# Kernel tuning notes

Measured on AMD Instinct MI355X. Metric: run time of the kernel, lower is better.

The kernel has to match this reference:

```python
import jax, jax.numpy as jnp
import numpy as np

NTOKEN, NINP, NHID = 50257, 256, 256
B, T = 64, 2048
RES, FC1 = 10, NHID // 3
EPS = 1e-5

def lrelu(x, p=0.01):
    return jnp.maximum(x, x * p)

def setup_inputs() -> dict:
    key = jax.random.key(0)
    ks = jax.random.split(key, 12)
    s = 0.05
    inp = {
        "input": jax.random.randint(ks[0], (B, T), 0, NTOKEN),
        "hx": jnp.zeros((B, NHID), jnp.float32),
        "cx": jnp.zeros((B, NHID), jnp.float32),
        "seq_len": jax.random.randint(ks[1], (B,), 1, T + 1),  # lengths in [1, T]
        "emb_w": jax.random.uniform(ks[2], (NTOKEN, NINP), jnp.float32, -0.1, 0.1),
        "W_ih": jax.random.normal(ks[3], (4 * NHID, NINP), jnp.float32) * s,
        "W_hh": jax.random.normal(ks[4], (4 * NHID, NHID), jnp.float32) * s,
        "b_ih": jnp.zeros((4 * NHID,), jnp.float32),
        "b_hh": jnp.zeros((4 * NHID,), jnp.float32),
        "rfc1_w": jax.random.normal(ks[5], (RES, NHID), jnp.float32) * s,
        "rfc1_b": jnp.zeros((RES,), jnp.float32),
        "rbn_g": jnp.ones((RES,), jnp.float32),
        "rbn_b": jnp.zeros((RES,), jnp.float32),
        "rbn_rm": jnp.zeros((RES,), jnp.float32),
        "rbn_rv": jnp.ones((RES,), jnp.float32),
        "rfc2_w": jax.random.normal(ks[6], (NHID, RES), jnp.float32) * s,
        "rfc2_b": jnp.zeros((NHID,), jnp.float32),
        "fc1_w": jax.random.normal(ks[7], (FC1, NHID), jnp.float32) * s,
        "fc1_b": jnp.zeros((FC1,), jnp.float32),
        "bn1_g": jnp.ones((FC1,), jnp.float32),
        "bn1_b": jnp.zeros((FC1,), jnp.float32),
        "bn1_rm": jnp.zeros((FC1,), jnp.float32),
        "bn1_rv": jnp.ones((FC1,), jnp.float32),
        "fc2_w": jax.random.normal(ks[8], (2, FC1), jnp.float32) * s,
        "fc2_b": jnp.zeros((2,), jnp.float32),
    }
    return inp

def reference(input, hx, cx, seq_len, emb_w, W_ih, W_hh, b_ih, b_hh,
              rfc1_w, rfc1_b, rbn_g, rbn_b, rbn_rm, rbn_rv, rfc2_w, rfc2_b,
              fc1_w, fc1_b, bn1_g, bn1_b, bn1_rm, bn1_rv, fc2_w, fc2_b):
    # eval mode: dropout = identity, noise = 0, BatchNorm uses running stats
    emb = emb_w[input.T]  # [T, B, ninp]
    # precompute input-side gates once (batched matmul) -> [T, B, 4*nhid]
    x_gates = jnp.einsum('tbi,gi->tbg', emb, W_ih) + b_ih + b_hh

    def step(carry, xg):
        h, c = carry
        gates = xg + h @ W_hh.T
        i, f, g, o = jnp.split(gates, 4, axis=-1)
        c = jax.nn.sigmoid(f) * c + jax.nn.sigmoid(i) * jnp.tanh(g)
        h = jax.nn.sigmoid(o) * jnp.tanh(c)
        return (h, c), h

    (hx_f, cx_f), outs = jax.lax.scan(step, (hx, cx), x_gates)  # outs: [T, B, nhid]

    # ragged mean pooling over first seq_len[b] steps
    mask = (jnp.arange(T)[:, None] < seq_len[None, :]).astype(outs.dtype)  # [T, B]
    feature = jnp.einsum('tbh,tb->bh', outs, mask) / seq_len[:, None].astype(outs.dtype)

    # ResNet block (eval)
    res = jax.nn.relu(feature) @ rfc1_w.T + rfc1_b
    res = jax.nn.relu(res)
    res = (res - rbn_rm) * jax.lax.rsqrt(rbn_rv + EPS) * rbn_g + rbn_b
    feature = feature + res @ rfc2_w.T + rfc2_b

    # classifier head
    fc = feature @ fc1_w.T + fc1_b
    fc = (fc - bn1_rm) * jax.lax.rsqrt(bn1_rv + EPS) * bn1_g + bn1_b
    fc = lrelu(fc)
    logits = fc @ fc2_w.T + fc2_b
    logp = jax.nn.log_softmax(logits, axis=-1)
    return (logp, hx_f, cx_f)
```

## Files before the change

kernel.cpp:

```cpp
#include <hip/hip_runtime.h>
#include <cstdint>


#define NTOKEN 50257
#define NINP 256
#define NHID 256
#define BB 64
#define TT 2048
#define NRES 10
#define NFC1 85
#define EPSV 1e-5f

typedef _Float16 f16;
typedef _Float16 f16x2 __attribute__((ext_vector_type(2)));
typedef _Float16 f16x8 __attribute__((ext_vector_type(8)));
typedef float f32x4 __attribute__((ext_vector_type(4)));

static __device__ __forceinline__ float sigm(float x) { return 1.0f / (1.0f + __expf(-x)); }
static __device__ __forceinline__ float tanh_(float x) {
  float ax = fabsf(x);
  float e = __expf(-2.0f * ax);
  float t = (1.0f - e) / (1.0f + e);
  return x < 0.0f ? -t : t;
}

static __device__ __forceinline__ float fdot2(f16x2 a, f16x2 b, float c) {
#if __has_builtin(__builtin_amdgcn_fdot2)
  return __builtin_amdgcn_fdot2(a, b, c, false);
#else
  return c + (float)a[0] * (float)b[0] + (float)a[1] * (float)b[1];
#endif
}

__global__ void k0_convert(const float* __restrict__ emb_w, const float* __restrict__ W_ih,
                           const float* __restrict__ b_ih, const float* __restrict__ b_hh,
                           f16* __restrict__ emb16, f16* __restrict__ wih16,
                           float* __restrict__ bias) {
  int64_t i = (int64_t)blockIdx.x * blockDim.x + threadIdx.x;
  if (i < (int64_t)NTOKEN * NINP) emb16[i] = (f16)emb_w[i];
  if (i < 4 * NHID * NINP) wih16[i] = (f16)W_ih[i];
  if (i < 4 * NHID) bias[i] = b_ih[i] + b_hh[i];
}

__global__ __launch_bounds__(256) void k1_gemm(const f16* __restrict__ emb16,
                                               const f16* __restrict__ wih16,
                                               const float* __restrict__ bias,
                                               f16* __restrict__ xgtab) {
  __shared__ __align__(16) f16 a_lds[64][40];
  __shared__ __align__(16) f16 b_lds[256][40];
  const int mt = blockIdx.x;
  const int nt0 = blockIdx.y * 256;
  const int tid = threadIdx.x;
  const int lane = tid & 63;
  const int w = tid >> 6;
  const int quad = lane >> 4;
  const int l16 = lane & 15;

  f32x4 acc[16];
#pragma unroll
  for (int i = 0; i < 16; i++) acc[i] = (f32x4){0.f, 0.f, 0.f, 0.f};

  const int ar = tid >> 2;
  int av = mt * 64 + ar;
  if (av > NTOKEN - 1) av = NTOKEN - 1;
  const int ac = (tid & 3) * 8;

  for (int kb = 0; kb < 256; kb += 32) {
    *(uint4*)&a_lds[ar][ac] = *(const uint4*)&emb16[av * 256 + kb + ac];
    {
      const uint4* bs = (const uint4*)&wih16[(nt0 + tid) * 256 + kb];
      uint4* bd = (uint4*)&b_lds[tid][0];
      bd[0] = bs[0]; bd[1] = bs[1]; bd[2] = bs[2]; bd[3] = bs[3];
    }
    __syncthreads();
    f16x8 af = *(const f16x8*)&a_lds[w * 16 + l16][quad * 8];
#pragma unroll
    for (int nt = 0; nt < 16; nt++) {
      f16x8 bf = *(const f16x8*)&b_lds[nt * 16 + l16][quad * 8];
      acc[nt] = __builtin_amdgcn_mfma_f32_16x16x32_f16(af, bf, acc[nt], 0, 0, 0);
    }
    __syncthreads();
  }
#pragma unroll
  for (int nt = 0; nt < 16; nt++) {
#pragma unroll
    for (int rg = 0; rg < 4; rg++) {
      int v = mt * 64 + w * 16 + quad * 4 + rg;
      if (v < NTOKEN) {
        int n = nt0 + nt * 16 + l16;
        xgtab[v * 1024 + n] = (f16)(acc[nt][rg] + bias[n]);
      }
    }
  }
}

#define RK 92
#define LK 36
__global__ __launch_bounds__(512, 2) void k2_rnn(
    const int* __restrict__ input, const float* __restrict__ hx0,
    const float* __restrict__ cx0, const int* __restrict__ seq_len,
    const float* __restrict__ Whh, const f16* __restrict__ xgtab,
    float* __restrict__ feat, float* __restrict__ out_hx, float* __restrict__ out_cx) {
  __shared__ uint2 lw2[LK * 512];
  __shared__ __align__(16) f16 hpak[NHID];
  __shared__ float fo_f[NHID];
  __shared__ float fo_o[NHID];

  const int b = blockIdx.x;
  const int tid = threadIdx.x;
  const int r0 = tid, r1 = tid + 512;

  unsigned int w0[RK], w1[RK];
#pragma unroll
  for (int m = 0; m < 128; m++) {
    float2 a = *(const float2*)&Whh[r0 * 256 + 2 * m];
    float2 d = *(const float2*)&Whh[r1 * 256 + 2 * m];
    f16x2 pa; pa[0] = (f16)a.x; pa[1] = (f16)a.y;
    f16x2 pd; pd[0] = (f16)d.x; pd[1] = (f16)d.y;
    unsigned int ua = __builtin_bit_cast(unsigned int, pa);
    unsigned int ud = __builtin_bit_cast(unsigned int, pd);
    if (m < RK) { w0[m] = ua; w1[m] = ud; }
    else { lw2[(m - RK) * 512 + tid] = make_uint2(ua, ud); }
  }

  float c = 0.0f, pool = 0.0f, hnew = 0.0f;
  if (tid < NHID) {
    hpak[tid] = (f16)hx0[b * NHID + tid];
    c = cx0[b * NHID + tid];
  }
  const int L = seq_len[b];
  __syncthreads();

  const int* tokp = input + b * TT;
  int tok_next = tokp[1];
  f16 xga, xgb;
  {
    int tok0 = tokp[0];
    xga = xgtab[tok0 * 1024 + r0];
    xgb = xgtab[tok0 * 1024 + r1];
  }

  for (int t = 0; t < TT; t++) {
    int tn = (t + 2 < TT) ? tokp[t + 2] : 0;
    f16 pfa = xgtab[tok_next * 1024 + r0];
    f16 pfb = xgtab[tok_next * 1024 + r1];

    float acc0 = (float)xga, acc1 = (float)xgb;
    const uint4* hp = (const uint4*)hpak;
#pragma unroll
    for (int mb = 0; mb < 32; mb++) {
      uint4 h4 = hp[mb];
#pragma unroll
      for (int j = 0; j < 4; j++) {
        const int m = mb * 4 + j;
        unsigned int hu = (j == 0) ? h4.x : (j == 1) ? h4.y : (j == 2) ? h4.z : h4.w;
        f16x2 hh = __builtin_bit_cast(f16x2, hu);
        f16x2 wa, wb;
        if (m < RK) {
          wa = __builtin_bit_cast(f16x2, w0[m]);
          wb = __builtin_bit_cast(f16x2, w1[m]);
        } else {
          uint2 ww = lw2[(m - RK) * 512 + tid];
          wa = __builtin_bit_cast(f16x2, ww.x);
          wb = __builtin_bit_cast(f16x2, ww.y);
        }
        acc0 = fdot2(wa, hh, acc0);
        acc1 = fdot2(wb, hh, acc1);
      }
    }

    if (tid >= NHID) {
      fo_f[tid - NHID] = sigm(acc0);
      fo_o[tid - NHID] = sigm(acc1);
    }
    __syncthreads();
    if (tid < NHID) {
      float ig = sigm(acc0);
      float gg = tanh_(acc1);
      c = fo_f[tid] * c + ig * gg;
      hnew = fo_o[tid] * tanh_(c);
      if (t < L) pool += hnew;
      hpak[tid] = (f16)hnew;
    }
    __syncthreads();
    xga = pfa; xgb = pfb; tok_next = tn;
  }

  if (tid < NHID) {
    feat[b * NHID + tid] = pool / (float)L;
    out_hx[b * NHID + tid] = hnew;
    out_cx[b * NHID + tid] = c;
  }
}

__global__ __launch_bounds__(256) void k3_head(const float* __restrict__ feat,
    const float* __restrict__ rfc1_w, const float* __restrict__ rfc1_b,
    const float* __restrict__ rbn_g, const float* __restrict__ rbn_b,
    const float* __restrict__ rbn_rm, const float* __restrict__ rbn_rv,
    const float* __restrict__ rfc2_w, const float* __restrict__ rfc2_b,
    const float* __restrict__ fc1_w, const float* __restrict__ fc1_b,
    const float* __restrict__ bn1_g, const float* __restrict__ bn1_b,
    const float* __restrict__ bn1_rm, const float* __restrict__ bn1_rv,
    const float* __restrict__ fc2_w, const float* __restrict__ fc2_b,
    float* __restrict__ logp) {
  __shared__ float f[256];
  __shared__ float f2[256];
  __shared__ float res[16];
  __shared__ float fcv[96];
  const int b = blockIdx.x, tid = threadIdx.x;
  const int wv = tid >> 6, lane = tid & 63;
  f[tid] = feat[b * 256 + tid];
  __syncthreads();
  for (int r = wv; r < NRES; r += 4) {
    float p = 0.f;
#pragma unroll
    for (int j0 = 0; j0 < 4; j0++) {
      int j = lane * 4 + j0;
      p += fmaxf(f[j], 0.f) * rfc1_w[r * 256 + j];
    }
    for (int off = 32; off > 0; off >>= 1) p += __shfl_down(p, off);
    if (lane == 0) {
      float x = p + rfc1_b[r];
      x = fmaxf(x, 0.f);
      x = (x - rbn_rm[r]) * rsqrtf(rbn_rv[r] + EPSV) * rbn_g[r] + rbn_b[r];
      res[r] = x;
    }
  }
  __syncthreads();
  {
    float s = rfc2_b[tid];
#pragma unroll
    for (int r = 0; r < NRES; r++) s += res[r] * rfc2_w[tid * NRES + r];
    f2[tid] = f[tid] + s;
  }
  __syncthreads();
  for (int o = wv; o < NFC1; o += 4) {
    float p = 0.f;
#pragma unroll
    for (int j0 = 0; j0 < 4; j0++) {
      int j = lane * 4 + j0;
      p += f2[j] * fc1_w[o * 256 + j];
    }
    for (int off = 32; off > 0; off >>= 1) p += __shfl_down(p, off);
    if (lane == 0) {
      float x = p + fc1_b[o];
      x = (x - bn1_rm[o]) * rsqrtf(bn1_rv[o] + EPSV) * bn1_g[o] + bn1_b[o];
      x = fmaxf(x, 0.01f * x);
      fcv[o] = x;
    }
  }
  __syncthreads();
  if (tid == 0) {
    float l0 = fc2_b[0], l1 = fc2_b[1];
    for (int o2 = 0; o2 < NFC1; o2++) {
      l0 += fcv[o2] * fc2_w[o2];
      l1 += fcv[o2] * fc2_w[NFC1 + o2];
    }
    float mx = fmaxf(l0, l1);
    float lse = mx + __logf(__expf(l0 - mx) + __expf(l1 - mx));
    logp[b * 2 + 0] = l0 - lse;
    logp[b * 2 + 1] = l1 - lse;
  }
}

extern "C" void kernel_launch(void* const* d_in, const int* in_sizes, int n_in,
                              void* d_out, int out_size, void* d_ws, size_t ws_size,
                              hipStream_t stream) {
  const int*   input  = (const int*)  d_in[0];
  const float* hx     = (const float*)d_in[1];
  const float* cx     = (const float*)d_in[2];
  const int*   seqlen = (const int*)  d_in[3];
  const float* emb_w  = (const float*)d_in[4];
  const float* W_ih   = (const float*)d_in[5];
  const float* W_hh   = (const float*)d_in[6];
  const float* b_ih   = (const float*)d_in[7];
  const float* b_hh   = (const float*)d_in[8];
  const float* rfc1_w = (const float*)d_in[9];
  const float* rfc1_b = (const float*)d_in[10];
  const float* rbn_g  = (const float*)d_in[11];
  const float* rbn_b  = (const float*)d_in[12];
  const float* rbn_rm = (const float*)d_in[13];
  const float* rbn_rv = (const float*)d_in[14];
  const float* rfc2_w = (const float*)d_in[15];
  const float* rfc2_b = (const float*)d_in[16];
  const float* fc1_w  = (const float*)d_in[17];
  const float* fc1_b  = (const float*)d_in[18];
  const float* bn1_g  = (const float*)d_in[19];
  const float* bn1_b  = (const float*)d_in[20];
  const float* bn1_rm = (const float*)d_in[21];
  const float* bn1_rv = (const float*)d_in[22];
  const float* fc2_w  = (const float*)d_in[23];
  const float* fc2_b  = (const float*)d_in[24];

  char* ws = (char*)d_ws;
  f16*   emb16 = (f16*)(ws);
  f16*   wih16 = (f16*)(ws + 25731584);
  float* bias  = (float*)(ws + 26255872);
  f16*   xgtab = (f16*)(ws + 26259968);
  float* feat  = (float*)(ws + 129186304);

  float* out = (float*)d_out;

  k0_convert<<<dim3(NTOKEN), 256, 0, stream>>>(emb_w, W_ih, b_ih, b_hh, emb16, wih16, bias);
  k1_gemm<<<dim3((NTOKEN + 63) / 64, 4), 256, 0, stream>>>(emb16, wih16, bias, xgtab);
  k2_rnn<<<dim3(BB), 512, 0, stream>>>(input, hx, cx, seqlen, W_hh, xgtab, feat,
                                       out + 128, out + 128 + BB * NHID);
  k3_head<<<dim3(BB), 256, 0, stream>>>(feat, rfc1_w, rfc1_b, rbn_g, rbn_b, rbn_rm, rbn_rv,
                                        rfc2_w, rfc2_b, fc1_w, fc1_b, bn1_g, bn1_b, bn1_rm,
                                        bn1_rv, fc2_w, fc2_b, out);
}
```

Measured before the change: 4.141 ms.

## Remap LSTM gate rows so gate exchange uses wave shuffles, double-buffer hidden state

The recurrent kernel now assigns rows so that each wave's lower half holds the i/g gates and its upper half the f/o gates of the same hidden units. The gate combination then uses cross-lane shuffles instead of shared-memory staging, and one of the two per-step barriers goes away. The hidden state is double-buffered, more W_hh columns are kept in registers (RK raised from 92 to 100), LDS weights are read as 128-bit vectors, and h loads are software-prefetched. The cost is higher register pressure, which the waves_per_eu attribute tries to contain, and half the threads sit idle during the cell update.

```diff
diff --git a/kernel.cpp b/kernel.cpp
--- a/kernel.cpp
+++ b/kernel.cpp
@@ -94,23 +94,28 @@
   }
 }
 
-#define RK 92
-#define LK 36
-__global__ __launch_bounds__(512, 2) void k2_rnn(
+#define RK 100
+#define LKW ((128 - RK) / 2)
+__global__ __attribute__((amdgpu_flat_work_group_size(512, 512), amdgpu_waves_per_eu(2, 2)))
+void k2_rnn(
     const int* __restrict__ input, const float* __restrict__ hx0,
     const float* __restrict__ cx0, const int* __restrict__ seq_len,
     const float* __restrict__ Whh, const f16* __restrict__ xgtab,
     float* __restrict__ feat, float* __restrict__ out_hx, float* __restrict__ out_cx) {
-  __shared__ uint2 lw2[LK * 512];
-  __shared__ __align__(16) f16 hpak[NHID];
-  __shared__ float fo_f[NHID];
-  __shared__ float fo_o[NHID];
+  __shared__ uint4 lw4[LKW * 512];
+  __shared__ __align__(16) f16 hpak[2][NHID];
 
   const int b = blockIdx.x;
   const int tid = threadIdx.x;
-  const int r0 = tid, r1 = tid + 512;
+  const int w = tid >> 6;
+  const int lane = tid & 63;
+  const int half = lane >> 5;
+  const int p = w * 32 + (lane & 31);
+  const int r0 = half ? (p + 256) : p;
+  const int r1 = half ? (p + 768) : (p + 512);
 
   unsigned int w0[RK], w1[RK];
+  unsigned int pa0 = 0, pd0 = 0;
 #pragma unroll
   for (int m = 0; m < 128; m++) {
     float2 a = *(const float2*)&Whh[r0 * 256 + 2 * m];
@@ -119,15 +124,18 @@
     f16x2 pd; pd[0] = (f16)d.x; pd[1] = (f16)d.y;
     unsigned int ua = __builtin_bit_cast(unsigned int, pa);
     unsigned int ud = __builtin_bit_cast(unsigned int, pd);
-    if (m < RK) { w0[m] = ua; w1[m] = ud; }
-    else { lw2[(m - RK) * 512 + tid] = make_uint2(ua, ud); }
+    if (m < RK) {
+      w0[m] = ua; w1[m] = ud;
+    } else if (((m - RK) & 1) == 0) {
+      pa0 = ua; pd0 = ud;
+    } else {
+      lw4[((m - RK) >> 1) * 512 + tid] = make_uint4(pa0, pd0, ua, ud);
+    }
   }
 
   float c = 0.0f, pool = 0.0f, hnew = 0.0f;
-  if (tid < NHID) {
-    hpak[tid] = (f16)hx0[b * NHID + tid];
-    c = cx0[b * NHID + tid];
-  }
+  if (tid < NHID) hpak[0][tid] = (f16)hx0[b * NHID + tid];
+  if (!half) c = cx0[b * NHID + p];
   const int L = seq_len[b];
   __syncthreads();
 
@@ -141,15 +149,25 @@
   }
 
   for (int t = 0; t < TT; t++) {
+    const int cur = t & 1;
     int tn = (t + 2 < TT) ? tokp[t + 2] : 0;
     f16 pfa = xgtab[tok_next * 1024 + r0];
     f16 pfb = xgtab[tok_next * 1024 + r1];
 
     float acc0 = (float)xga, acc1 = (float)xgb;
-    const uint4* hp = (const uint4*)hpak;
+    const uint4* hp = (const uint4*)hpak[cur];
+    uint4 hC = hp[0];
+    uint4 hN = hp[1];
 #pragma unroll
     for (int mb = 0; mb < 32; mb++) {
-      uint4 h4 = hp[mb];
+      uint4 h4 = hC;
+      hC = hN;
+      if (mb < 30) hN = hp[mb + 2];
+      uint4 ww0, ww1;
+      if (4 * mb >= RK) {
+        ww0 = lw4[(2 * (mb - RK / 4)) * 512 + tid];
+        ww1 = lw4[(2 * (mb - RK / 4) + 1) * 512 + tid];
+      }
 #pragma unroll
       for (int j = 0; j < 4; j++) {
         const int m = mb * 4 + j;
@@ -160,36 +178,36 @@
           wa = __builtin_bit_cast(f16x2, w0[m]);
           wb = __builtin_bit_cast(f16x2, w1[m]);
         } else {
-          uint2 ww = lw2[(m - RK) * 512 + tid];
-          wa = __builtin_bit_cast(f16x2, ww.x);
-          wb = __builtin_bit_cast(f16x2, ww.y);
+          unsigned int uwa = (j == 0) ? ww0.x : (j == 1) ? ww0.z : (j == 2) ? ww1.x : ww1.z;
+          unsigned int uwb = (j == 0) ? ww0.y : (j == 1) ? ww0.w : (j == 2) ? ww1.y : ww1.w;
+          wa = __builtin_bit_cast(f16x2, uwa);
+          wb = __builtin_bit_cast(f16x2, uwb);
         }
         acc0 = fdot2(wa, hh, acc0);
         acc1 = fdot2(wb, hh, acc1);
       }
     }
 
-    if (tid >= NHID) {
-      fo_f[tid - NHID] = sigm(acc0);
-      fo_o[tid - NHID] = sigm(acc1);
-    }
-    __syncthreads();
-    if (tid < NHID) {
-      float ig = sigm(acc0);
+    float s0 = sigm(acc0);
+    float oa = 0.0f;
+    if (half) oa = sigm(acc1);
+    float fs = __shfl_xor(half ? s0 : 0.0f, 32);
+    float os = __shfl_xor(oa, 32);
+    if (!half) {
       float gg = tanh_(acc1);
-      c = fo_f[tid] * c + ig * gg;
-      hnew = fo_o[tid] * tanh_(c);
+      c = fs * c + s0 * gg;
+      hnew = os * tanh_(c);
       if (t < L) pool += hnew;
-      hpak[tid] = (f16)hnew;
+      hpak[cur ^ 1][p] = (f16)hnew;
     }
     __syncthreads();
     xga = pfa; xgb = pfb; tok_next = tn;
   }
 
-  if (tid < NHID) {
-    feat[b * NHID + tid] = pool / (float)L;
-    out_hx[b * NHID + tid] = hnew;
-    out_cx[b * NHID + tid] = c;
+  if (!half) {
+    feat[b * NHID + p] = pool / (float)L;
+    out_hx[b * NHID + p] = hnew;
+    out_cx[b * NHID + p] = c;
   }
 }
 
```

New measurement: 3.936 ms. 1.05x faster.

## Compute LSTM recurrent matvec with MFMA and permuted gate-table layout

Applied to the files above, without the earlier changes.

Replaces the per-thread fdot2 recurrent matvec with MFMA 16x16x32 instructions. W_hh fragments are split across registers, LDS and per-step global reloads, and the hidden state sits in a double-buffered LDS vector fed into row 0 of the A operand. The GEMM output table is permuted so each lane gets its four gates for a hidden unit together. This drops one barrier per step and moves the gate math onto the matrix units, but wastes 15/16 of each MFMA and re-reads part of W_hh from global memory every timestep.

```diff
diff --git a/kernel.cpp b/kernel.cpp
--- a/kernel.cpp
+++ b/kernel.cpp
@@ -13,6 +13,7 @@
 
 typedef _Float16 f16;
 typedef _Float16 f16x2 __attribute__((ext_vector_type(2)));
+typedef _Float16 f16x4 __attribute__((ext_vector_type(4)));
 typedef _Float16 f16x8 __attribute__((ext_vector_type(8)));
 typedef float f32x4 __attribute__((ext_vector_type(4)));
 
@@ -22,14 +23,6 @@
   float e = __expf(-2.0f * ax);
   float t = (1.0f - e) / (1.0f + e);
   return x < 0.0f ? -t : t;
-}
-
-static __device__ __forceinline__ float fdot2(f16x2 a, f16x2 b, float c) {
-#if __has_builtin(__builtin_amdgcn_fdot2)
-  return __builtin_amdgcn_fdot2(a, b, c, false);
-#else
-  return c + (float)a[0] * (float)b[0] + (float)a[1] * (float)b[1];
-#endif
 }
 
 __global__ void k0_convert(const float* __restrict__ emb_w, const float* __restrict__ W_ih,
@@ -40,6 +33,11 @@
   if (i < (int64_t)NTOKEN * NINP) emb16[i] = (f16)emb_w[i];
   if (i < 4 * NHID * NINP) wih16[i] = (f16)W_ih[i];
   if (i < 4 * NHID) bias[i] = b_ih[i] + b_hh[i];
+}
+
+__global__ void k0b_whh(const float* __restrict__ Whh, f16* __restrict__ whh16) {
+  int i = blockIdx.x * 256 + threadIdx.x;
+  if (i < 4 * NHID * NHID) whh16[i] = (f16)Whh[i];
 }
 
 __global__ __launch_bounds__(256) void k1_gemm(const f16* __restrict__ emb16,
@@ -88,108 +86,138 @@
       int v = mt * 64 + w * 16 + quad * 4 + rg;
       if (v < NTOKEN) {
         int n = nt0 + nt * 16 + l16;
-        xgtab[v * 1024 + n] = (f16)(acc[nt][rg] + bias[n]);
+        xgtab[v * 1024 + nt * 64 + l16 * 4 + blockIdx.y] = (f16)(acc[nt][rg] + bias[n]);
       }
     }
   }
 }
 
-#define RK 92
-#define LK 36
-__global__ __launch_bounds__(512, 2) void k2_rnn(
-    const int* __restrict__ input, const float* __restrict__ hx0,
-    const float* __restrict__ cx0, const int* __restrict__ seq_len,
-    const float* __restrict__ Whh, const f16* __restrict__ xgtab,
-    float* __restrict__ feat, float* __restrict__ out_hx, float* __restrict__ out_cx) {
-  __shared__ uint2 lw2[LK * 512];
-  __shared__ __align__(16) f16 hpak[NHID];
-  __shared__ float fo_f[NHID];
-  __shared__ float fo_o[NHID];
+__global__ __attribute__((amdgpu_flat_work_group_size(512, 512), amdgpu_waves_per_eu(2, 2)))
+void k2_rnn(const int* __restrict__ input, const float* __restrict__ hx0,
+            const float* __restrict__ cx0, const int* __restrict__ seq_len,
+            const f16* __restrict__ whh16, const f16* __restrict__ xgtab,
+            float* __restrict__ feat, float* __restrict__ out_hx,
+            float* __restrict__ out_cx) {
+  __shared__ __align__(16) f16 wlds[8][16][64][8];
+  __shared__ __align__(16) f16 hbuf[2][256];
 
   const int b = blockIdx.x;
   const int tid = threadIdx.x;
-  const int r0 = tid, r1 = tid + 512;
-
-  unsigned int w0[RK], w1[RK];
-#pragma unroll
-  for (int m = 0; m < 128; m++) {
-    float2 a = *(const float2*)&Whh[r0 * 256 + 2 * m];
-    float2 d = *(const float2*)&Whh[r1 * 256 + 2 * m];
-    f16x2 pa; pa[0] = (f16)a.x; pa[1] = (f16)a.y;
-    f16x2 pd; pd[0] = (f16)d.x; pd[1] = (f16)d.y;
-    unsigned int ua = __builtin_bit_cast(unsigned int, pa);
-    unsigned int ud = __builtin_bit_cast(unsigned int, pd);
-    if (m < RK) { w0[m] = ua; w1[m] = ud; }
-    else { lw2[(m - RK) * 512 + tid] = make_uint2(ua, ud); }
-  }
-
-  float c = 0.0f, pool = 0.0f, hnew = 0.0f;
-  if (tid < NHID) {
-    hpak[tid] = (f16)hx0[b * NHID + tid];
-    c = cx0[b * NHID + tid];
+  const int w = tid >> 6;
+  const int lane = tid & 63;
+  const int quad = lane >> 4;
+  const int l16 = lane & 15;
+
+  const int goff = (w * 32 + l16) * 256 + quad * 8;
+
+  f16x8 wreg[40];
+#pragma unroll
+  for (int nt = 0; nt < 8; ++nt) {
+    const int g = nt >> 1, hh = nt & 1;
+    const f16* rp = whh16 + (g * 256 + hh * 16) * 256 + goff;
+#pragma unroll
+    for (int ks = 0; ks < 7; ++ks) {
+      f16x8 fr = *(const f16x8*)(rp + ks * 32);
+      if (ks < 5) wreg[nt * 5 + ks] = fr;
+      else *(f16x8*)&wlds[w][(ks - 5) * 8 + nt][lane][0] = fr;
+    }
+  }
+
+  float cst[2] = {0.f, 0.f}, pool2[2] = {0.f, 0.f}, hlast[2] = {0.f, 0.f};
+  if (quad == 0) {
+#pragma unroll
+    for (int hh = 0; hh < 2; ++hh) {
+      const int n = w * 32 + hh * 16 + l16;
+      hbuf[0][n] = (f16)hx0[b * 256 + n];
+      cst[hh] = cx0[b * 256 + n];
+    }
   }
   const int L = seq_len[b];
-  __syncthreads();
-
   const int* tokp = input + b * TT;
-  int tok_next = tokp[1];
-  f16 xga, xgb;
+  int tok1 = tokp[1];
+  uint2 xgc_raw[2] = {{0u, 0u}, {0u, 0u}};
+  uint2 xgn_raw[2] = {{0u, 0u}, {0u, 0u}};
   {
-    int tok0 = tokp[0];
-    xga = xgtab[tok0 * 1024 + r0];
-    xgb = xgtab[tok0 * 1024 + r1];
-  }
-
-  for (int t = 0; t < TT; t++) {
-    int tn = (t + 2 < TT) ? tokp[t + 2] : 0;
-    f16 pfa = xgtab[tok_next * 1024 + r0];
-    f16 pfb = xgtab[tok_next * 1024 + r1];
-
-    float acc0 = (float)xga, acc1 = (float)xgb;
-    const uint4* hp = (const uint4*)hpak;
-#pragma unroll
-    for (int mb = 0; mb < 32; mb++) {
-      uint4 h4 = hp[mb];
-#pragma unroll
-      for (int j = 0; j < 4; j++) {
-        const int m = mb * 4 + j;
-        unsigned int hu = (j == 0) ? h4.x : (j == 1) ? h4.y : (j == 2) ? h4.z : h4.w;
-        f16x2 hh = __builtin_bit_cast(f16x2, hu);
-        f16x2 wa, wb;
-        if (m < RK) {
-          wa = __builtin_bit_cast(f16x2, w0[m]);
-          wb = __builtin_bit_cast(f16x2, w1[m]);
-        } else {
-          uint2 ww = lw2[(m - RK) * 512 + tid];
-          wa = __builtin_bit_cast(f16x2, ww.x);
-          wb = __builtin_bit_cast(f16x2, ww.y);
-        }
-        acc0 = fdot2(wa, hh, acc0);
-        acc1 = fdot2(wb, hh, acc1);
+    const int tok0 = tokp[0];
+    if (quad == 0) {
+      const f16* xr = xgtab + (int64_t)tok0 * 1024 + w * 128 + l16 * 4;
+      xgc_raw[0] = *(const uint2*)xr;
+      xgc_raw[1] = *(const uint2*)(xr + 64);
+    }
+  }
+  __syncthreads();
+
+#pragma unroll 1
+  for (int t = 0; t < TT; ++t) {
+    const int cur = t & 1;
+
+    f16x8 g7[8];
+#pragma unroll
+    for (int nt = 0; nt < 8; ++nt) {
+      const int g = nt >> 1, hh = nt & 1;
+      g7[nt] = *(const f16x8*)(whh16 + (g * 256 + hh * 16) * 256 + 224 + goff);
+    }
+
+    const int tok2 = tokp[(t + 2 < TT) ? (t + 2) : (TT - 1)];
+    if (quad == 0) {
+      const f16* xr = xgtab + (int64_t)tok1 * 1024 + w * 128 + l16 * 4;
+      xgn_raw[0] = *(const uint2*)xr;
+      xgn_raw[1] = *(const uint2*)(xr + 64);
+    }
+
+    f32x4 acc[8];
+#pragma unroll
+    for (int nt = 0; nt < 8; ++nt) {
+      const int g = nt >> 1, hh = nt & 1;
+      float v = 0.f;
+      if (quad == 0) v = (float)(__builtin_bit_cast(f16x4, xgc_raw[hh])[g]);
+      acc[nt][0] = v; acc[nt][1] = 0.f; acc[nt][2] = 0.f; acc[nt][3] = 0.f;
+    }
+
+#pragma unroll
+    for (int ks = 0; ks < 8; ++ks) {
+      f16x8 af;
+#pragma unroll
+      for (int z = 0; z < 8; ++z) af[z] = (f16)0;
+      if (l16 == 0) af = *(const f16x8*)&hbuf[cur][ks * 32 + quad * 8];
+#pragma unroll
+      for (int nt = 0; nt < 8; ++nt) {
+        f16x8 bf;
+        if (ks < 5) bf = wreg[nt * 5 + ks];
+        else if (ks < 7) bf = *(const f16x8*)&wlds[w][(ks - 5) * 8 + nt][lane][0];
+        else bf = g7[nt];
+        acc[nt] = __builtin_amdgcn_mfma_f32_16x16x32_f16(af, bf, acc[nt], 0, 0, 0);
       }
     }
 
-    if (tid >= NHID) {
-      fo_f[tid - NHID] = sigm(acc0);
-      fo_o[tid - NHID] = sigm(acc1);
-    }
+    if (quad == 0) {
+#pragma unroll
+      for (int hh = 0; hh < 2; ++hh) {
+        const float iv = sigm(acc[0 + hh][0]);
+        const float fv = sigm(acc[2 + hh][0]);
+        const float gv = tanh_(acc[4 + hh][0]);
+        const float ov = sigm(acc[6 + hh][0]);
+        const float cc = fv * cst[hh] + iv * gv;
+        cst[hh] = cc;
+        const float hv = ov * tanh_(cc);
+        hlast[hh] = hv;
+        if (t < L) pool2[hh] += hv;
+        hbuf[cur ^ 1][w * 32 + hh * 16 + l16] = (f16)hv;
+      }
+    }
+    xgc_raw[0] = xgn_raw[0]; xgc_raw[1] = xgn_raw[1];
+    tok1 = tok2;
     __syncthreads();
-    if (tid < NHID) {
-      float ig = sigm(acc0);
-      float gg = tanh_(acc1);
-      c = fo_f[tid] * c + ig * gg;
-      hnew = fo_o[tid] * tanh_(c);
-      if (t < L) pool += hnew;
-      hpak[tid] = (f16)hnew;
-    }
-    __syncthreads();
-    xga = pfa; xgb = pfb; tok_next = tn;
-  }
-
-  if (tid < NHID) {
-    feat[b * NHID + tid] = pool / (float)L;
-    out_hx[b * NHID + tid] = hnew;
-    out_cx[b * NHID + tid] = c;
+  }
+
+  if (quad == 0) {
+#pragma unroll
+    for (int hh = 0; hh < 2; ++hh) {
+      const int n = w * 32 + hh * 16 + l16;
+      feat[b * 256 + n] = pool2[hh] / (float)L;
+      out_hx[b * 256 + n] = hlast[hh];
+      out_cx[b * 256 + n] = cst[hh];
+    }
   }
 }
 
@@ -294,6 +322,7 @@
 
   char* ws = (char*)d_ws;
   f16*   emb16 = (f16*)(ws);
+  f16*   whh16 = (f16*)(ws);
   f16*   wih16 = (f16*)(ws + 25731584);
   float* bias  = (float*)(ws + 26255872);
   f16*   xgtab = (f16*)(ws + 26259968);
@@ -303,7 +332,8 @@
 
   k0_convert<<<dim3(NTOKEN), 256, 0, stream>>>(emb_w, W_ih, b_ih, b_hh, emb16, wih16, bias);
   k1_gemm<<<dim3((NTOKEN + 63) / 64, 4), 256, 0, stream>>>(emb16, wih16, bias, xgtab);
-  k2_rnn<<<dim3(BB), 512, 0, stream>>>(input, hx, cx, seqlen, W_hh, xgtab, feat,
+  k0b_whh<<<dim3((4 * NHID * NHID + 255) / 256), 256, 0, stream>>>(W_hh, whh16);
+  k2_rnn<<<dim3(BB), 512, 0, stream>>>(input, hx, cx, seqlen, whh16, xgtab, feat,
                                        out + 128, out + 128 + BB * NHID);
   k3_head<<<dim3(BB), 256, 0, stream>>>(feat, rfc1_w, rfc1_b, rbn_g, rbn_b, rbn_rm, rbn_rv,
                                         rfc2_w, rfc2_b, fc1_w, fc1_b, bn1_g, bn1_b, bn1_rm,
```

Result: slower. 4.977 ms (+20.2%).
